# Performance work log

Measured on AMD Instinct MI355X. Metric: run time of the kernel, lower is better.

## Reference

```python
import jax, jax.numpy as jnp
import numpy as np

NUM_NODES = 1_000_000
D_IN = 128
D_OUT = 128
NUM_REL = 16          # relations; +1 for self-connection relation
BATCH = 16384
NUM_SAMPLE = 32


def setup_inputs() -> dict:
    key = jax.random.key(0)
    k1, k2, k3, k4 = jax.random.split(key, 4)
    embed_table = jax.random.normal(k1, (NUM_NODES, D_IN), dtype=jnp.float32)
    # per-relation weight: [R+1, size_out, size_in], xavier-ish scale
    relation_weights = jax.random.normal(k2, (NUM_REL + 1, D_OUT, D_IN), dtype=jnp.float32)
    relation_weights = relation_weights * jnp.sqrt(2.0 / (D_IN + D_OUT))
    sampled_neighbors = jax.random.randint(k3, (BATCH, NUM_SAMPLE), 0, NUM_NODES, dtype=jnp.int64)
    sampled_relations = jax.random.randint(k4, (BATCH, NUM_SAMPLE), 0, NUM_REL + 1, dtype=jnp.int64)
    return {
        "embed_table": embed_table,
        "relation_weights": relation_weights,
        "sampled_neighbors": sampled_neighbors,
        "sampled_relations": sampled_relations,
    }


def reference(embed_table, relation_weights, sampled_neighbors, sampled_relations):
    # Gather sampled neighbor embeddings: [N, S, D]
    emb = embed_table[sampled_neighbors]
    num_sample = emb.shape[1]
    num_rel_p1 = relation_weights.shape[0]
    # One-hot relation mask [N, S, R+1]; aggregated = mean over S of (emb * onehot)
    # Equivalent einsum avoids materializing the [N, S, R+1, D] intermediate.
    onehot = jax.nn.one_hot(sampled_relations, num_rel_p1, dtype=emb.dtype)
    agg = jnp.einsum("nsr,nsd->nrd", onehot, emb) / num_sample  # [N, R+1, D]
    # Per-relation matmul (bmm over R+1) then mean over relations.
    # relation_weights: [R+1, O, I]; agg: [N, R+1, I] -> [N, O]
    out = jnp.einsum("nri,roi->no", agg, relation_weights) / num_rel_p1
    return jax.nn.relu(out * 1000.0)
```

## Files before the change

### kernel.cpp

```cpp
#include <hip/hip_runtime.h>

constexpr int D     = 128;
constexpr int R1    = 17;
constexpr int BATCH = 16384;
constexpr int S     = 32;
constexpr int K     = R1 * D;
constexpr int KB    = K / 8;
constexpr int NPB   = 16;
constexpr int NGRP  = 4;
constexpr int AS    = K + 8;
constexpr int THREADS = 1024;
constexpr int GRID  = BATCH / (NPB * NGRP);

typedef __attribute__((ext_vector_type(8))) short short8;
typedef __attribute__((ext_vector_type(4))) float f32x4;

__device__ __forceinline__ unsigned short f2bf_u(float f) {
    union { float f; unsigned u; } c; c.f = f;
    unsigned u = c.u;
    u += 0x7fffu + ((u >> 16) & 1u);
    return (unsigned short)(u >> 16);
}
__device__ __forceinline__ unsigned pack2bf(float lo, float hi) {
    return (unsigned)f2bf_u(lo) | ((unsigned)f2bf_u(hi) << 16);
}

__global__ void pack_w_kernel(const float* __restrict__ W, short* __restrict__ Bp) {
    int tid = blockIdx.x * 256 + threadIdx.x;
    if (tid >= R1 * D * D) return;
    int og = tid / K;
    int k  = tid - og * K;
    int r = k >> 7, i = k & 127;
    float v = W[((size_t)r * D + og) * D + i];
    int ot = og >> 4, o = og & 15, kb = k >> 3, j = k & 7;
    Bp[(((size_t)ot * KB + kb) * 16 + o) * 8 + j] = (short)f2bf_u(v);
}

#define ACC_SWITCH(rr_, vv_)                                          \
    switch (rr_) {                                                    \
        case 0:  a0.x  += vv_.x; a0.y  += vv_.y; break;               \
        case 1:  a1.x  += vv_.x; a1.y  += vv_.y; break;               \
        case 2:  a2.x  += vv_.x; a2.y  += vv_.y; break;               \
        case 3:  a3.x  += vv_.x; a3.y  += vv_.y; break;               \
        case 4:  a4.x  += vv_.x; a4.y  += vv_.y; break;               \
        case 5:  a5.x  += vv_.x; a5.y  += vv_.y; break;               \
        case 6:  a6.x  += vv_.x; a6.y  += vv_.y; break;               \
        case 7:  a7.x  += vv_.x; a7.y  += vv_.y; break;               \
        case 8:  a8.x  += vv_.x; a8.y  += vv_.y; break;               \
        case 9:  a9.x  += vv_.x; a9.y  += vv_.y; break;               \
        case 10: a10.x += vv_.x; a10.y += vv_.y; break;               \
        case 11: a11.x += vv_.x; a11.y += vv_.y; break;               \
        case 12: a12.x += vv_.x; a12.y += vv_.y; break;               \
        case 13: a13.x += vv_.x; a13.y += vv_.y; break;               \
        case 14: a14.x += vv_.x; a14.y += vv_.y; break;               \
        case 15: a15.x += vv_.x; a15.y += vv_.y; break;               \
        default: a16.x += vv_.x; a16.y += vv_.y; break;               \
    }

__device__ __forceinline__ void gather_one(const float* __restrict__ embed,
                                           const int*   __restrict__ nbrs,
                                           const int*   __restrict__ rels,
                                           int gn, int lane, short* row)
{
    int my;
    if (lane < 32) my = nbrs[(size_t)gn * S + lane];
    else           my = rels[(size_t)gn * S + (lane - 32)];

    float2 a0={0,0},a1={0,0},a2={0,0},a3={0,0},a4={0,0},a5={0,0},
           a6={0,0},a7={0,0},a8={0,0},a9={0,0},a10={0,0},a11={0,0},
           a12={0,0},a13={0,0},a14={0,0},a15={0,0},a16={0,0};

    #pragma unroll 1
    for (int c = 0; c < 2; ++c) {
        const int sbase = c * 16;
        float2 v[16];
        #pragma unroll
        for (int j = 0; j < 16; ++j) {
            const int idx = __builtin_amdgcn_readlane(my, sbase + j);
            v[j] = *reinterpret_cast<const float2*>(embed + (size_t)idx * D + 2 * lane);
        }
        #pragma unroll
        for (int j = 0; j < 16; ++j) {
            const int r = __builtin_amdgcn_readlane(my, 32 + sbase + j);
            const float2 vx = v[j];
            ACC_SWITCH(r, vx)
        }
    }

    unsigned* arow_ = reinterpret_cast<unsigned*>(row) + lane;
    arow_[0*64]  = pack2bf(a0.x,  a0.y);   arow_[1*64]  = pack2bf(a1.x,  a1.y);
    arow_[2*64]  = pack2bf(a2.x,  a2.y);   arow_[3*64]  = pack2bf(a3.x,  a3.y);
    arow_[4*64]  = pack2bf(a4.x,  a4.y);   arow_[5*64]  = pack2bf(a5.x,  a5.y);
    arow_[6*64]  = pack2bf(a6.x,  a6.y);   arow_[7*64]  = pack2bf(a7.x,  a7.y);
    arow_[8*64]  = pack2bf(a8.x,  a8.y);   arow_[9*64]  = pack2bf(a9.x,  a9.y);
    arow_[10*64] = pack2bf(a10.x, a10.y);  arow_[11*64] = pack2bf(a11.x, a11.y);
    arow_[12*64] = pack2bf(a12.x, a12.y);  arow_[13*64] = pack2bf(a13.x, a13.y);
    arow_[14*64] = pack2bf(a14.x, a14.y);  arow_[15*64] = pack2bf(a15.x, a15.y);
    arow_[16*64] = pack2bf(a16.x, a16.y);
}

__global__ __launch_bounds__(THREADS, 4)
void rgcn_pc_kernel(const float* __restrict__ embed,
                    const short* __restrict__ Bp,
                    const int*   __restrict__ nbrs,
                    const int*   __restrict__ rels,
                    float* __restrict__ out)
{
    __shared__ short At[2][NPB][AS];

    const int t     = threadIdx.x;
    const int lane  = t & 63;
    const int w     = t >> 6;
    const int base0 = blockIdx.x * NGRP * NPB;

    if (w < 8) {
        #pragma unroll 1
        for (int p = 0; p < 2; ++p)
            gather_one(embed, nbrs, rels, base0 + 2 * w + p, lane, &At[0][2 * w + p][0]);
    }
    __syncthreads();

    #pragma unroll 1
    for (int g = 0; g < NGRP; ++g) {
        if (w < 8) {
            if (g + 1 < NGRP) {
                const int nb = base0 + (g + 1) * NPB;
                #pragma unroll 1
                for (int p = 0; p < 2; ++p)
                    gather_one(embed, nbrs, rels, nb + 2 * w + p, lane,
                               &At[(g + 1) & 1][2 * w + p][0]);
            }
        } else {
            const int cw  = w - 8;
            const int m   = lane & 15;
            const int kb4 = lane >> 4;

            f32x4 acc = {0.f, 0.f, 0.f, 0.f};
            const short* ar = &At[g & 1][m][kb4 * 8];
            const short* bb = Bp + (((size_t)cw * KB + kb4) * 16 + m) * 8;

            #pragma unroll 4
            for (int step = 0; step < K / 32; ++step) {
                const short8 a = *reinterpret_cast<const short8*>(ar + step * 32);
                const short8 b = *reinterpret_cast<const short8*>(bb + (size_t)step * 512);
                acc = __builtin_amdgcn_mfma_f32_16x16x32_bf16(a, b, acc, 0, 0, 0);
            }

            const float sc = 1000.0f / (float)(S * R1);
            const int nbase = base0 + g * NPB;
            #pragma unroll
            for (int j = 0; j < 4; ++j) {
                out[(size_t)(nbase + kb4 * 4 + j) * D + cw * 16 + m] =
                    fmaxf(acc[j] * sc, 0.0f);
            }
        }
        __syncthreads();
    }
}

extern "C" void kernel_launch(void* const* d_in, const int* in_sizes, int n_in,
                              void* d_out, int out_size, void* d_ws, size_t ws_size,
                              hipStream_t stream) {
    const float* embed = (const float*)d_in[0];
    const float* W     = (const float*)d_in[1];
    const int*   nbrs  = (const int*)d_in[2];
    const int*   rels  = (const int*)d_in[3];
    float* out = (float*)d_out;
    short* Bp  = (short*)d_ws;

    hipLaunchKernelGGL(pack_w_kernel, dim3((R1 * D * D + 255) / 256), dim3(256), 0, stream,
                       W, Bp);
    hipLaunchKernelGGL(rgcn_pc_kernel, dim3(GRID), dim3(THREADS), 0, stream,
                       embed, Bp, nbrs, rels, out);
}
```

Measured before the change: 97.50 us.

## Interleave gather with MFMA in compute warps and prefetch neighbor ids

Before this change, 8 warps did the gathering and 8 warps ran the GEMM. Now all 16 warps gather one node each. The 8 GEMM warps split their MFMA loop into quarters and put embedding loads and relation accumulation for their own node between the quarters. Neighbor and relation ids are prefetched two groups ahead, and the final barrier is dropped. The aim is to hide gather latency behind MFMA work and use the idle GEMM warps for gathering, at the cost of more register pressure in the mixed warps.

Result: slower. 249.8 us (+156.2%).

```diff
diff --git a/kernel.cpp b/kernel.cpp
--- a/kernel.cpp
+++ b/kernel.cpp
@@ -8,9 +8,11 @@
 constexpr int KB    = K / 8;
 constexpr int NPB   = 16;
 constexpr int NGRP  = 4;
-constexpr int AS    = K + 8;
+constexpr int ASH   = K + 8;
 constexpr int THREADS = 1024;
 constexpr int GRID  = BATCH / (NPB * NGRP);
+constexpr int NSTEP = K / 32;
+constexpr int QSTEP = NSTEP / 4;
 
 typedef __attribute__((ext_vector_type(8))) short short8;
 typedef __attribute__((ext_vector_type(4))) float f32x4;
@@ -57,19 +59,53 @@
         default: a16.x += vv_.x; a16.y += vv_.y; break;               \
     }
 
-__device__ __forceinline__ void gather_one(const float* __restrict__ embed,
-                                           const int*   __restrict__ nbrs,
-                                           const int*   __restrict__ rels,
-                                           int gn, int lane, short* row)
-{
-    int my;
-    if (lane < 32) my = nbrs[(size_t)gn * S + lane];
-    else           my = rels[(size_t)gn * S + (lane - 32)];
-
+#define LOAD8(buf, myreg, sbase)                                                \
+    { _Pragma("unroll") for (int j = 0; j < 8; ++j) {                           \
+        const int idx_ = __builtin_amdgcn_readlane(myreg, (sbase) + j);         \
+        buf[j] = *reinterpret_cast<const float2*>(                              \
+            embed + (size_t)idx_ * D + 2 * lane); } }
+
+#define ACC8(myreg, sbase, buf)                                                 \
+    { _Pragma("unroll") for (int j = 0; j < 8; ++j) {                           \
+        const int rsel_ = __builtin_amdgcn_readlane(myreg, 32 + (sbase) + j);   \
+        const float2 vsel_ = buf[j];                                            \
+        ACC_SWITCH(rsel_, vsel_) } }
+
+#define ZERO_ACC()                                                              \
+    a0={0,0};a1={0,0};a2={0,0};a3={0,0};a4={0,0};a5={0,0};a6={0,0};a7={0,0};    \
+    a8={0,0};a9={0,0};a10={0,0};a11={0,0};a12={0,0};a13={0,0};a14={0,0};        \
+    a15={0,0};a16={0,0};
+
+#define STORE_ACCP(ptr)                                                         \
+    { unsigned* arow_ = reinterpret_cast<unsigned*>(ptr) + lane;                \
+      arow_[0*64]=pack2bf(a0.x,a0.y);   arow_[1*64]=pack2bf(a1.x,a1.y);         \
+      arow_[2*64]=pack2bf(a2.x,a2.y);   arow_[3*64]=pack2bf(a3.x,a3.y);         \
+      arow_[4*64]=pack2bf(a4.x,a4.y);   arow_[5*64]=pack2bf(a5.x,a5.y);         \
+      arow_[6*64]=pack2bf(a6.x,a6.y);   arow_[7*64]=pack2bf(a7.x,a7.y);         \
+      arow_[8*64]=pack2bf(a8.x,a8.y);   arow_[9*64]=pack2bf(a9.x,a9.y);         \
+      arow_[10*64]=pack2bf(a10.x,a10.y);arow_[11*64]=pack2bf(a11.x,a11.y);      \
+      arow_[12*64]=pack2bf(a12.x,a12.y);arow_[13*64]=pack2bf(a13.x,a13.y);      \
+      arow_[14*64]=pack2bf(a14.x,a14.y);arow_[15*64]=pack2bf(a15.x,a15.y);      \
+      arow_[16*64]=pack2bf(a16.x,a16.y); }
+
+#define GEMM17(q_)                                                              \
+    { _Pragma("unroll") for (int s = (q_)*QSTEP; s < (q_)*QSTEP + QSTEP; ++s) { \
+        const short8 afrag_ = *reinterpret_cast<const short8*>(ar + s * 32);    \
+        const short8 bfrag_ = *reinterpret_cast<const short8*>(bb + (size_t)s * 512); \
+        acc = __builtin_amdgcn_mfma_f32_16x16x32_bf16(afrag_, bfrag_, acc, 0, 0, 0); } }
+
+__device__ __forceinline__ int load_ids(const int* __restrict__ nbrs,
+                                        const int* __restrict__ rels,
+                                        int gn, int lane) {
+    return (lane < 32) ? nbrs[(size_t)gn * S + lane]
+                       : rels[(size_t)gn * S + (lane - 32)];
+}
+
+__device__ __forceinline__ void gather_full(const float* __restrict__ embed,
+                                            int my, int lane, short* rowp) {
     float2 a0={0,0},a1={0,0},a2={0,0},a3={0,0},a4={0,0},a5={0,0},
            a6={0,0},a7={0,0},a8={0,0},a9={0,0},a10={0,0},a11={0,0},
            a12={0,0},a13={0,0},a14={0,0},a15={0,0},a16={0,0};
-
     #pragma unroll 1
     for (int c = 0; c < 2; ++c) {
         const int sbase = c * 16;
@@ -86,75 +122,78 @@
             ACC_SWITCH(r, vx)
         }
     }
-
-    unsigned* arow_ = reinterpret_cast<unsigned*>(row) + lane;
-    arow_[0*64]  = pack2bf(a0.x,  a0.y);   arow_[1*64]  = pack2bf(a1.x,  a1.y);
-    arow_[2*64]  = pack2bf(a2.x,  a2.y);   arow_[3*64]  = pack2bf(a3.x,  a3.y);
-    arow_[4*64]  = pack2bf(a4.x,  a4.y);   arow_[5*64]  = pack2bf(a5.x,  a5.y);
-    arow_[6*64]  = pack2bf(a6.x,  a6.y);   arow_[7*64]  = pack2bf(a7.x,  a7.y);
-    arow_[8*64]  = pack2bf(a8.x,  a8.y);   arow_[9*64]  = pack2bf(a9.x,  a9.y);
-    arow_[10*64] = pack2bf(a10.x, a10.y);  arow_[11*64] = pack2bf(a11.x, a11.y);
-    arow_[12*64] = pack2bf(a12.x, a12.y);  arow_[13*64] = pack2bf(a13.x, a13.y);
-    arow_[14*64] = pack2bf(a14.x, a14.y);  arow_[15*64] = pack2bf(a15.x, a15.y);
-    arow_[16*64] = pack2bf(a16.x, a16.y);
+    STORE_ACCP(rowp)
 }
 
 __global__ __launch_bounds__(THREADS, 4)
-void rgcn_pc_kernel(const float* __restrict__ embed,
-                    const short* __restrict__ Bp,
-                    const int*   __restrict__ nbrs,
-                    const int*   __restrict__ rels,
-                    float* __restrict__ out)
+void rgcn_kernel(const float* __restrict__ embed,
+                 const short* __restrict__ Bp,
+                 const int*   __restrict__ nbrs,
+                 const int*   __restrict__ rels,
+                 float* __restrict__ out)
 {
-    __shared__ short At[2][NPB][AS];
+    __shared__ short At[2][NPB][ASH];
 
     const int t     = threadIdx.x;
     const int lane  = t & 63;
     const int w     = t >> 6;
     const int base0 = blockIdx.x * NGRP * NPB;
 
-    if (w < 8) {
-        #pragma unroll 1
-        for (int p = 0; p < 2; ++p)
-            gather_one(embed, nbrs, rels, base0 + 2 * w + p, lane, &At[0][2 * w + p][0]);
-    }
+    {
+        const int id0 = load_ids(nbrs, rels, base0 + w, lane);
+        gather_full(embed, id0, lane, &At[0][w][0]);
+    }
+    int my = load_ids(nbrs, rels, base0 + NPB + w, lane);
     __syncthreads();
+
+    const float sc = 1000.0f / (float)(S * R1);
 
     #pragma unroll 1
     for (int g = 0; g < NGRP; ++g) {
+        const int buf   = g & 1;
+        const int gbase = base0 + g * NPB;
+
         if (w < 8) {
-            if (g + 1 < NGRP) {
-                const int nb = base0 + (g + 1) * NPB;
-                #pragma unroll 1
-                for (int p = 0; p < 2; ++p)
-                    gather_one(embed, nbrs, rels, nb + 2 * w + p, lane,
-                               &At[(g + 1) & 1][2 * w + p][0]);
+            const int m   = lane & 15;
+            const int kb4 = lane >> 4;
+            const short* ar = &At[buf][m][kb4 * 8];
+            const short* bb = Bp + (((size_t)w * KB + kb4) * 16 + m) * 8;
+            f32x4 acc = {0.f, 0.f, 0.f, 0.f};
+
+            if (g < NGRP - 1) {
+                int my2 = 0;
+                if (g < NGRP - 2)
+                    my2 = load_ids(nbrs, rels, base0 + (g + 2) * NPB + w, lane);
+                float2 a0,a1,a2,a3,a4,a5,a6,a7,a8,a9,a10,a11,a12,a13,a14,a15,a16;
+                ZERO_ACC();
+                float2 vA[8], vB[8];
+                GEMM17(0) LOAD8(vA, my, 0)
+                GEMM17(1) LOAD8(vB, my, 8)  ACC8(my, 0,  vA)
+                GEMM17(2) LOAD8(vA, my, 16) ACC8(my, 8,  vB)
+                GEMM17(3) LOAD8(vB, my, 24) ACC8(my, 16, vA)
+                ACC8(my, 24, vB)
+                STORE_ACCP(&At[buf ^ 1][w][0])
+                my = my2;
+            } else {
+                GEMM17(0) GEMM17(1) GEMM17(2) GEMM17(3)
+            }
+
+            #pragma unroll
+            for (int j = 0; j < 4; ++j) {
+                out[(size_t)(gbase + kb4 * 4 + j) * D + w * 16 + m] =
+                    fmaxf(acc[j] * sc, 0.0f);
             }
         } else {
-            const int cw  = w - 8;
-            const int m   = lane & 15;
-            const int kb4 = lane >> 4;
-
-            f32x4 acc = {0.f, 0.f, 0.f, 0.f};
-            const short* ar = &At[g & 1][m][kb4 * 8];
-            const short* bb = Bp + (((size_t)cw * KB + kb4) * 16 + m) * 8;
-
-            #pragma unroll 4
-            for (int step = 0; step < K / 32; ++step) {
-                const short8 a = *reinterpret_cast<const short8*>(ar + step * 32);
-                const short8 b = *reinterpret_cast<const short8*>(bb + (size_t)step * 512);
-                acc = __builtin_amdgcn_mfma_f32_16x16x32_bf16(a, b, acc, 0, 0, 0);
-            }
-
-            const float sc = 1000.0f / (float)(S * R1);
-            const int nbase = base0 + g * NPB;
-            #pragma unroll
-            for (int j = 0; j < 4; ++j) {
-                out[(size_t)(nbase + kb4 * 4 + j) * D + cw * 16 + m] =
-                    fmaxf(acc[j] * sc, 0.0f);
+            if (g < NGRP - 1) {
+                int my2 = 0;
+                if (g < NGRP - 2)
+                    my2 = load_ids(nbrs, rels, base0 + (g + 2) * NPB + w, lane);
+                gather_full(embed, my, lane, &At[buf ^ 1][w][0]);
+                my = my2;
             }
         }
-        __syncthreads();
+
+        if (g < NGRP - 1) __syncthreads();
     }
 }
 
@@ -170,6 +209,6 @@
 
     hipLaunchKernelGGL(pack_w_kernel, dim3((R1 * D * D + 255) / 256), dim3(256), 0, stream,
                        W, Bp);
-    hipLaunchKernelGGL(rgcn_pc_kernel, dim3(GRID), dim3(THREADS), 0, stream,
+    hipLaunchKernelGGL(rgcn_kernel, dim3(GRID), dim3(THREADS), 0, stream,
                        embed, Bp, nbrs, rels, out);
 }
```
